# Performance work log

Hardware: AMD Instinct MI355X
Metric: run time of the kernel (lower is better)

## Reference

```python
import jax, jax.numpy as jnp
import numpy as np

EMBED_DIMS = 256
NUM_GROUPS = 8
NUM_LEVELS = 4
NUM_CAMS = 6
NUM_LEARNABLE_PTS = 6
FIX_SCALE = np.array([[0,0,0],[0.45,0,0],[-0.45,0,0],[0,0.45,0],[0,-0.45,0],[0,0,0.45],[0,0,-0.45]], dtype=np.float32)
NUM_PTS = len(FIX_SCALE) + NUM_LEARNABLE_PTS  # 13
GROUP_DIMS = EMBED_DIMS // NUM_GROUPS


def safe_sigmoid(x):
    return jax.nn.sigmoid(jnp.clip(x, -9.21, 9.21))


def get_rotation_matrix(q):
    # q: [..., 4] quaternion (w, x, y, z), normalized first (GaussianFormer convention)
    q = q / jnp.linalg.norm(q, axis=-1, keepdims=True)
    w, x, y, z = q[..., 0], q[..., 1], q[..., 2], q[..., 3]
    R = jnp.stack([
        jnp.stack([1 - 2 * (y * y + z * z), 2 * (x * y - w * z), 2 * (x * z + w * y)], axis=-1),
        jnp.stack([2 * (x * y + w * z), 1 - 2 * (x * x + z * z), 2 * (y * z - w * x)], axis=-1),
        jnp.stack([2 * (x * z - w * y), 2 * (y * z + w * x), 1 - 2 * (x * x + y * y)], axis=-1),
    ], axis=-2)
    return R  # [..., 3, 3]


def key_points_generator(anchor, instance_feature, W_learn, b_learn):
    bs, num_anchor = anchor.shape[:2]
    fix_scale = jnp.asarray(FIX_SCALE, anchor.dtype)  # [7, 3]
    scale = jnp.broadcast_to(fix_scale[None, None], (bs, num_anchor, fix_scale.shape[0], 3))
    learnable = safe_sigmoid((instance_feature @ W_learn + b_learn)
                             .reshape(bs, num_anchor, NUM_LEARNABLE_PTS, 3)) - 0.5
    scale = jnp.concatenate([scale, learnable], axis=-2)         # [bs, na, P, 3]
    gs_scales = anchor[..., None, 3:6]                           # [bs, na, 1, 3]
    key_points = scale * gs_scales                               # [bs, na, P, 3]
    rot_T = jnp.swapaxes(get_rotation_matrix(anchor[..., 6:10]), -1, -2)  # [bs, na, 3, 3]
    key_points = jnp.einsum('bnij,bnpj->bnpi', rot_T, key_points)
    return key_points + anchor[..., None, :3]                    # [bs, na, P, 3]


def project_points(key_points, projection_mat, image_wh):
    # key_points [bs, na, P, 3], projection_mat [bs, cams, 4, 4]
    ones = jnp.ones_like(key_points[..., :1])
    pts4 = jnp.concatenate([key_points, ones], axis=-1)          # [bs, na, P, 4]
    p2d = jnp.einsum('bcij,bnpj->bcnpi', projection_mat, pts4)   # [bs, cams, na, P, 4]
    p2d = p2d[..., :2] / jnp.maximum(p2d[..., 2:3], 1e-5)
    p2d = p2d / image_wh[:, :, None, None]
    return jnp.clip(p2d, 0.0, 0.9999)                            # [bs, cams, na, P, 2]


def bilinear_sample(feat, pts):
    # feat [bs, cams, C, H, W], pts [bs, P, cams, 2] normalized to [0,1]
    bs, cams, C, H, W = feat.shape
    x = pts[..., 0] * W - 0.5
    y = pts[..., 1] * H - 0.5
    x0 = jnp.floor(x); y0 = jnp.floor(y)
    wx = x - x0; wy = y - y0
    x0i = x0.astype(jnp.int32); y0i = y0.astype(jnp.int32)
    feat_f = jnp.transpose(feat, (0, 1, 3, 4, 2)).reshape(bs, cams, H * W, C)
    b_idx = jnp.arange(bs)[:, None, None]
    c_idx = jnp.arange(cams)[None, None, :]

    def gather(yy, xx):
        valid = (yy >= 0) & (yy < H) & (xx >= 0) & (xx < W)
        yc = jnp.clip(yy, 0, H - 1)
        xc = jnp.clip(xx, 0, W - 1)
        v = feat_f[b_idx, c_idx, yc * W + xc]                    # [bs, P, cams, C]
        return v * valid[..., None].astype(v.dtype)

    v00 = gather(y0i, x0i)
    v01 = gather(y0i, x0i + 1)
    v10 = gather(y0i + 1, x0i)
    v11 = gather(y0i + 1, x0i + 1)
    wx = wx[..., None]; wy = wy[..., None]
    return (v00 * (1 - wx) * (1 - wy) + v01 * wx * (1 - wy)
            + v10 * (1 - wx) * wy + v11 * wx * wy)               # [bs, P, cams, C]


def deformable_aggregate(feature_maps, points_2d, weights):
    # points_2d [bs, P, cams, 2]; weights [bs, P, cams, levels, groups]
    bs, P = points_2d.shape[:2]
    out = jnp.zeros((bs, P, NUM_GROUPS, GROUP_DIMS), points_2d.dtype)
    for l, feat in enumerate(feature_maps):
        samp = bilinear_sample(feat, points_2d)                  # [bs, P, cams, C]
        samp = samp.reshape(bs, P, feat.shape[1], NUM_GROUPS, GROUP_DIMS)
        out = out + jnp.einsum('bpcgd,bpcg->bpgd', samp, weights[:, :, :, l, :])
    return out.reshape(bs, P, EMBED_DIMS)


def _forward(pts3d, instance_feature, anchor, feat0, feat1, feat2, feat3,
             projection_mat, image_wh, W_learn, b_learn, W_wts, b_wts, W_out, b_out):
    bs, num_anchor = instance_feature.shape[:2]
    key_points = key_points_generator(anchor, instance_feature, W_learn, b_learn)
    # softmax weights over cams*levels*pts jointly, per group
    w = (instance_feature @ W_wts + b_wts).reshape(bs, num_anchor, -1, NUM_GROUPS)
    w = jax.nn.softmax(w, axis=-2)
    w = w.reshape(bs, num_anchor, NUM_CAMS, NUM_LEVELS, NUM_PTS, NUM_GROUPS)
    w = jnp.transpose(w, (0, 1, 4, 2, 3, 5)).reshape(bs, num_anchor * NUM_PTS, NUM_CAMS, NUM_LEVELS, NUM_GROUPS)
    p2d = project_points(key_points, projection_mat, image_wh)   # [bs, cams, na, P, 2]
    p2d = jnp.transpose(p2d, (0, 2, 3, 1, 4)).reshape(bs, num_anchor * NUM_PTS, NUM_CAMS, 2)
    feats = deformable_aggregate([feat0, feat1, feat2, feat3], p2d, w)
    feats = feats.reshape(bs, num_anchor, NUM_PTS, EMBED_DIMS).sum(axis=2)
    output = feats @ W_out + b_out
    return output + instance_feature


def setup_inputs() -> dict:
    key = jax.random.key(0)
    ks = jax.random.split(key, 16)
    bs, na = 1, 4096
    shapes = [(bs, 6, 256, 64, 176), (bs, 6, 256, 32, 88), (bs, 6, 256, 16, 44), (bs, 6, 256, 8, 22)]
    inp = {
        'pts3d': jax.random.normal(ks[0], (100000, 3), jnp.float32),
        'instance_feature': jax.random.normal(ks[1], (bs, na, EMBED_DIMS), jnp.float32),
        'anchor': jax.random.normal(ks[2], (bs, na, 11), jnp.float32),
        'feat0': jax.random.normal(ks[3], shapes[0], jnp.float32),
        'feat1': jax.random.normal(ks[4], shapes[1], jnp.float32),
        'feat2': jax.random.normal(ks[5], shapes[2], jnp.float32),
        'feat3': jax.random.normal(ks[6], shapes[3], jnp.float32),
        'projection_mat': jax.random.normal(ks[7], (bs, NUM_CAMS, 4, 4), jnp.float32),
        'image_wh': jnp.broadcast_to(jnp.array([704.0, 256.0], jnp.float32), (bs, NUM_CAMS, 2)),
        'W_learn': jax.random.normal(ks[8], (EMBED_DIMS, NUM_LEARNABLE_PTS * 3), jnp.float32) * 0.02,
        'b_learn': jnp.zeros((NUM_LEARNABLE_PTS * 3,), jnp.float32),
        'W_wts': jax.random.normal(ks[9], (EMBED_DIMS, NUM_GROUPS * NUM_CAMS * NUM_LEVELS * NUM_PTS), jnp.float32) * 0.02,
        'b_wts': jnp.zeros((NUM_GROUPS * NUM_CAMS * NUM_LEVELS * NUM_PTS,), jnp.float32),
        'W_out': jax.random.normal(ks[10], (EMBED_DIMS, EMBED_DIMS), jnp.float32) * 0.02,
        'b_out': jnp.zeros((EMBED_DIMS,), jnp.float32),
    }
    return inp


def reference(pts3d, instance_feature, anchor, feat0, feat1, feat2, feat3,
              projection_mat, image_wh, W_learn, b_learn, W_wts, b_wts, W_out, b_out):
    return _forward(pts3d, instance_feature, anchor, feat0, feat1, feat2, feat3,
                    projection_mat, image_wh, W_learn, b_learn, W_wts, b_wts, W_out, b_out)
```

## Files before the change

### kernel.cpp

```cpp
#include <hip/hip_runtime.h>
#include <math.h>


#define FT_L0 0
#define FT_L1 17301504
#define FT_L2 21626880
#define FT_L3 22708224
#define WS_LOGB 5744640
#define WS_FEATB 10856448
#define WS_LEARN 11380736
#define WS_AB 11454464
#define WS_BB 11978752
#define WS_WOB 12306432
#define WS_BIASP 12339200

typedef float v2f __attribute__((ext_vector_type(2)));
typedef __attribute__((ext_vector_type(8))) short bf16x8;
typedef __attribute__((ext_vector_type(4))) float f32x4;

__device__ const float FIXS[7][3] = {
    {0.f, 0.f, 0.f},  {0.45f, 0.f, 0.f}, {-0.45f, 0.f, 0.f}, {0.f, 0.45f, 0.f},
    {0.f, -0.45f, 0.f}, {0.f, 0.f, 0.45f}, {0.f, 0.f, -0.45f}};

__device__ __forceinline__ unsigned int f2bf(float f) {
  unsigned int u = __float_as_uint(f);
  u += 0x7fffu + ((u >> 16) & 1u);
  return u >> 16;
}
__device__ __forceinline__ float bf2f(unsigned short u) {
  return __uint_as_float(((unsigned int)u) << 16);
}

__global__ __launch_bounds__(256) void k_stage(
    const float* __restrict__ f0, const float* __restrict__ f1,
    const float* __restrict__ f2, const float* __restrict__ f3,
    unsigned char* __restrict__ featF,
    const float* __restrict__ iw, const float* __restrict__ Ww,
    const float* __restrict__ Wl, const float* __restrict__ Wo,
    const float* __restrict__ b_wts,
    unsigned short* __restrict__ Ab, unsigned short* __restrict__ Bb,
    unsigned short* __restrict__ Wob, float* __restrict__ biasP) {
  __shared__ unsigned short smu[32][33];
  const int tid = threadIdx.x;
  const int bid = blockIdx.x;
  if (bid < 2688) {
    const int bx7 = bid % 7;
    const int y = (bid / 7) & 63;
    const int c = bid / 448;
    const float* src;
    unsigned char* dst;
    int H, W, xt;
    if (bx7 < 3)      { src = f0; dst = featF + FT_L0; H = 64; W = 176; xt = bx7 * 64; }
    else if (bx7 < 5) { src = f1; dst = featF + FT_L1; H = 32; W = 88;  xt = (bx7 - 3) * 64; }
    else if (bx7 < 6) { src = f2; dst = featF + FT_L2; H = 16; W = 44;  xt = 0; }
    else              { src = f3; dst = featF + FT_L3; H = 8;  W = 22;  xt = 0; }
    if (y >= H) return;
    const int x = xt + (tid & 31) * 2;
    if (x >= W) return;
    const int q8 = tid >> 5;
    const int HW = H * W;
    const float* sp = src + ((c * 256 + q8 * 32) * H + y) * W + x;
    float2 v[32];
#pragma unroll
    for (int k = 0; k < 32; ++k) v[k] = *(const float2*)(sp + k * HW);
    __builtin_amdgcn_sched_barrier(0);
    unsigned int r0[8], r1[8];
#pragma unroll
    for (int k8 = 0; k8 < 8; ++k8) {
      int pk = __builtin_amdgcn_cvt_pk_fp8_f32(v[k8 * 4 + 0].x, v[k8 * 4 + 1].x, 0, false);
      pk = __builtin_amdgcn_cvt_pk_fp8_f32(v[k8 * 4 + 2].x, v[k8 * 4 + 3].x, pk, true);
      r0[k8] = (unsigned int)pk;
      int pk1 = __builtin_amdgcn_cvt_pk_fp8_f32(v[k8 * 4 + 0].y, v[k8 * 4 + 1].y, 0, false);
      pk1 = __builtin_amdgcn_cvt_pk_fp8_f32(v[k8 * 4 + 2].y, v[k8 * 4 + 3].y, pk1, true);
      r1[k8] = (unsigned int)pk1;
    }
    unsigned char* drow = dst + (((c * H + y) * W + x) * 256) + q8 * 32;
    *(uint4*)(drow)            = make_uint4(r0[0], r0[1], r0[2], r0[3]);
    *(uint4*)(drow + 16)       = make_uint4(r0[4], r0[5], r0[6], r0[7]);
    *(uint4*)(drow + 256)      = make_uint4(r1[0], r1[1], r1[2], r1[3]);
    *(uint4*)(drow + 256 + 16) = make_uint4(r1[4], r1[5], r1[6], r1[7]);
    return;
  }
  const int bx = bid - 2688;
  if (bx < 1024) {
    const int i = bx * 256 + tid;
    const float4 v = ((const float4*)iw)[i];
    uint2 o;
    o.x = f2bf(v.x) | (f2bf(v.y) << 16);
    o.y = f2bf(v.z) | (f2bf(v.w) << 16);
    const int mtile = i >> 10;
    const int ml = (i >> 6) & 15;
    const int kk = (i & 63) >> 3;
    const int q = (i >> 1) & 3;
    const int jj = (i & 1) * 4;
    *(uint2*)&Ab[mtile * 4096 + kk * 512 + q * 128 + ml * 8 + jj] = o;
    return;
  }
  const int i = tid & 31;
  const int r = tid >> 5;
  const int bxb = bx - 1024;
  if (bxb < 640) {
    const int j0 = (bxb % 80) * 32;
    const int k0 = (bxb / 80) * 32;
#pragma unroll
    for (int rr = r; rr < 32; rr += 8) {
      const int k = k0 + rr, jc = j0 + i;
      float v = 0.f;
      if (jc < 2496) v = Ww[k * 2496 + jc];
      else if (jc < 2514) v = Wl[k * 18 + (jc - 2496)];
      smu[rr][i] = (unsigned short)f2bf(v);
    }
    __syncthreads();
    const int jn = tid >> 3;
    const int kq = tid & 7;
    const int jc = j0 + jn;
    if (jc < 2514) {
      int colp;
      if (jc < 2496) {
        const int g = jc & 7, s = jc >> 3;
        const int c = s / 52, r2 = s - c * 52;
        const int l = r2 / 13, p = r2 - l * 13;
        colp = g * 312 + (p * 6 + c) * 4 + l;
      } else {
        colp = jc;
      }
      const int k = k0 + kq * 4;
      const int ntile = colp >> 4, mln = colp & 15;
      const int kkn = k >> 5, qn = (k >> 3) & 3, jj = k & 7;
      unsigned int h0 = (unsigned int)smu[kq * 4 + 0][jn] |
                        ((unsigned int)smu[kq * 4 + 1][jn] << 16);
      unsigned int h1 = (unsigned int)smu[kq * 4 + 2][jn] |
                        ((unsigned int)smu[kq * 4 + 3][jn] << 16);
      *(uint2*)&Bb[ntile * 4096 + kkn * 512 + qn * 128 + mln * 8 + jj] =
          make_uint2(h0, h1);
    }
    return;
  }
  const int bxw = bxb - 640;
  if (bxw < 64) {
    const int j0 = (bxw & 7) * 32;
    const int k0 = (bxw >> 3) * 32;
#pragma unroll
    for (int rr = r; rr < 32; rr += 8)
      smu[rr][i] = (unsigned short)f2bf(Wo[(k0 + rr) * 256 + j0 + i]);
    __syncthreads();
#pragma unroll
    for (int rr = r; rr < 32; rr += 8)
      Wob[(j0 + rr) * 256 + k0 + i] = smu[i][rr];
    return;
  }
  {
    const int jcol = (bxw - 64) * 256 + tid;
    if (jcol < 2496) {
      const int g = jcol & 7, s = jcol >> 3;
      const int c = s / 52, r2 = s - c * 52;
      const int l = r2 / 13, p = r2 - l * 13;
      biasP[g * 312 + (p * 6 + c) * 4 + l] = b_wts[jcol];
    }
  }
}

__global__ __launch_bounds__(256) void k_wts_mfma(
    const unsigned short* __restrict__ Ab, const unsigned short* __restrict__ Bb,
    const float* __restrict__ biasP, const float* __restrict__ b_learn,
    unsigned short* __restrict__ logitsP, float* __restrict__ learn) {
  __shared__ __align__(16) unsigned short t64[64][88];
  const int tid = threadIdx.x;
  const int w = tid >> 6, lane = tid & 63;
  const int ml = lane & 15, q = lane >> 4;
  const int n0 = blockIdx.x * 64;
  const int m0 = blockIdx.y * 64;
  f32x4 acc[4] = {{0.f, 0.f, 0.f, 0.f}, {0.f, 0.f, 0.f, 0.f},
                  {0.f, 0.f, 0.f, 0.f}, {0.f, 0.f, 0.f, 0.f}};
  const unsigned short* Ap = Ab + (blockIdx.y * 4 + w) * 4096 + lane * 8;
  const unsigned short* Bp = Bb + blockIdx.x * 4 * 4096 + lane * 8;
#pragma unroll
  for (int kk = 0; kk < 8; ++kk) {
    const bf16x8 a = *(const bf16x8*)(Ap + kk * 512);
#pragma unroll
    for (int nt = 0; nt < 4; ++nt) {
      const bf16x8 b = *(const bf16x8*)(Bp + nt * 4096 + kk * 512);
      acc[nt] = __builtin_amdgcn_mfma_f32_16x16x32_bf16(a, b, acc[nt], 0, 0, 0);
    }
  }
  if (blockIdx.x < 39) {
    const int wr = w * 16 + q * 4;
#pragma unroll
    for (int nt = 0; nt < 4; ++nt) {
      const float b = biasP[n0 + nt * 16 + ml];
#pragma unroll
      for (int r = 0; r < 4; ++r)
        t64[wr + r][nt * 16 + ml] = (unsigned short)f2bf(acc[nt][r] + b);
    }
    __syncthreads();
    const int row = tid >> 2, cq = tid & 3;
    unsigned short* drow = logitsP + (m0 + row) * 2496 + n0;
    *(uint4*)(drow + cq * 8) = *(const uint4*)&t64[row][cq * 8];
    *(uint4*)(drow + 32 + cq * 8) = *(const uint4*)&t64[row][32 + cq * 8];
  } else {
    const int rowb = m0 + w * 16 + q * 4;
#pragma unroll
    for (int nt = 0; nt < 4; ++nt) {
      const int col = n0 + nt * 16 + ml;
      if (col < 2514) {
        const float b = b_learn[col - 2496];
#pragma unroll
        for (int r = 0; r < 4; ++r) {
          float v = fminf(fmaxf(acc[nt][r] + b, -9.21f), 9.21f);
          learn[(rowb + r) * 18 + (col - 2496)] = 1.f / (1.f + expf(-v)) - 0.5f;
        }
      }
    }
  }
}

__device__ __forceinline__ void fma16(const uint4 u, const float s, v2f* acc) {
  const v2f w = {s, s};
  acc[0] += __builtin_amdgcn_cvt_pk_f32_fp8((int)u.x, false) * w;
  acc[1] += __builtin_amdgcn_cvt_pk_f32_fp8((int)u.x, true) * w;
  acc[2] += __builtin_amdgcn_cvt_pk_f32_fp8((int)u.y, false) * w;
  acc[3] += __builtin_amdgcn_cvt_pk_f32_fp8((int)u.y, true) * w;
  acc[4] += __builtin_amdgcn_cvt_pk_f32_fp8((int)u.z, false) * w;
  acc[5] += __builtin_amdgcn_cvt_pk_f32_fp8((int)u.z, true) * w;
  acc[6] += __builtin_amdgcn_cvt_pk_f32_fp8((int)u.w, false) * w;
  acc[7] += __builtin_amdgcn_cvt_pk_f32_fp8((int)u.w, true) * w;
}

__global__ __launch_bounds__(256, 8) void k_sample(
    const float* __restrict__ anchor, const unsigned short* __restrict__ logitsP,
    const float* __restrict__ learn_g, const unsigned char* __restrict__ featF,
    const float* __restrict__ proj, const float* __restrict__ wh,
    unsigned short* __restrict__ featsB) {
  const int n = blockIdx.x;
  const int tid = threadIdx.x;
  const int lane = tid & 63;
  const int wave = tid >> 6;
  __shared__ __align__(16) unsigned short s_w[8 * 328];
  __shared__ float s_p2d[78][2];
  __shared__ float s_learn[18];
  __shared__ union SmpLds {
    struct { int4 off[320]; float4 wt[320]; } tab;
    float red[4][256];
  } u;

  {
    const uint4* lp = (const uint4*)(logitsP + (size_t)n * 2496);
    for (int i = tid; i < 312; i += 256) {
      const int g = i / 39;
      ((uint4*)s_w)[g * 41 + (i - g * 39)] = lp[i];
    }
  }
  if (tid < 64) s_w[(tid >> 3) * 328 + 312 + (tid & 7)] = 0;
  if (tid < 18) s_learn[tid] = learn_g[n * 18 + tid];
  __syncthreads();

#pragma unroll
  for (int gg = 0; gg < 2; ++gg) {
    unsigned short* row = &s_w[(wave * 2 + gg) * 328];
    float l[5];
    float mx = -1e30f;
#pragma unroll
    for (int i = 0; i < 5; ++i) {
      const int s = lane + i * 64;
      l[i] = (s < 312) ? bf2f(row[s]) : -1e30f;
      mx = fmaxf(mx, l[i]);
    }
    for (int off = 32; off; off >>= 1) mx = fmaxf(mx, __shfl_xor(mx, off));
    float sum = 0.f;
#pragma unroll
    for (int i = 0; i < 5; ++i) {
      l[i] = __expf(l[i] - mx);
      sum += l[i];
    }
    for (int off = 32; off; off >>= 1) sum += __shfl_xor(sum, off);
    const float inv = 1.f / sum;
#pragma unroll
    for (int i = 0; i < 5; ++i) {
      const int s = lane + i * 64;
      if (s < 312) row[s] = (unsigned short)f2bf(l[i] * inv);
    }
  }

  if (tid < 78) {
    const int p = tid / 6, c = tid % 6;
    const float* an = anchor + n * 11;
    float qw = an[6], qx = an[7], qy = an[8], qz = an[9];
    const float qinv = 1.f / sqrtf(qw * qw + qx * qx + qy * qy + qz * qz);
    qw *= qinv; qx *= qinv; qy *= qinv; qz *= qinv;
    const float R00 = 1.f - 2.f * (qy * qy + qz * qz), R01 = 2.f * (qx * qy - qw * qz), R02 = 2.f * (qx * qz + qw * qy);
    const float R10 = 2.f * (qx * qy + qw * qz), R11 = 1.f - 2.f * (qx * qx + qz * qz), R12 = 2.f * (qy * qz - qw * qx);
    const float R20 = 2.f * (qx * qz - qw * qy), R21 = 2.f * (qy * qz + qw * qx), R22 = 1.f - 2.f * (qx * qx + qy * qy);
    float s0, s1, s2;
    if (p < 7) {
      s0 = FIXS[p][0]; s1 = FIXS[p][1]; s2 = FIXS[p][2];
    } else {
      const int b = (p - 7) * 3;
      s0 = s_learn[b]; s1 = s_learn[b + 1]; s2 = s_learn[b + 2];
    }
    const float vx = s0 * an[3], vy = s1 * an[4], vz = s2 * an[5];
    const float kx = R00 * vx + R10 * vy + R20 * vz + an[0];
    const float ky = R01 * vx + R11 * vy + R21 * vz + an[1];
    const float kz = R02 * vx + R12 * vy + R22 * vz + an[2];
    const float* P = proj + c * 16;
    const float h0 = P[0] * kx + P[1] * ky + P[2] * kz + P[3];
    const float h1 = P[4] * kx + P[5] * ky + P[6] * kz + P[7];
    const float h2 = P[8] * kx + P[9] * ky + P[10] * kz + P[11];
    const float zz = fmaxf(h2, 1e-5f);
    float px = h0 / zz / wh[c * 2 + 0];
    float py = h1 / zz / wh[c * 2 + 1];
    px = fminf(fmaxf(px, 0.f), 0.9999f);
    py = fminf(fmaxf(py, 0.f), 0.9999f);
    s_p2d[tid][0] = px;
    s_p2d[tid][1] = py;
  }
  __syncthreads();

  {
    constexpr int LBB[4] = {FT_L0, FT_L1, FT_L2, FT_L3};
    constexpr int CSB[4] = {2883584, 720896, 180224, 45056};
    for (int t = tid; t < 320; t += 256) {
      const int pc = t >> 2, l = t & 3;
      if (pc >= 78) {
        u.tab.off[t] = make_int4(0, 0, 0, 0);
        u.tab.wt[t] = make_float4(0.f, 0.f, 0.f, 0.f);
        continue;
      }
      const int c = pc % 6;
      const int H = 64 >> l, W = 176 >> l;
      const float fx = s_p2d[pc][0] * (float)W - 0.5f;
      const float fy = s_p2d[pc][1] * (float)H - 0.5f;
      const float x0f = floorf(fx), y0f = floorf(fy);
      const float wx = fx - x0f, wy = fy - y0f;
      const int x0 = (int)x0f, y0 = (int)y0f;
      const float mx0 = (x0 >= 0) ? 1.f : 0.f;
      const float mx1 = (x0 + 1 < W) ? 1.f : 0.f;
      const float my0 = (y0 >= 0) ? 1.f : 0.f;
      const float my1 = (y0 + 1 < H) ? 1.f : 0.f;
      const int cx0 = max(x0, 0), cx1 = min(x0 + 1, W - 1);
      const int cy0 = max(y0, 0), cy1 = min(y0 + 1, H - 1);
      const int base = LBB[l] + c * CSB[l];
      int4 o;
      o.x = base + (cy0 * W + cx0) * 256;
      o.y = base + (cy0 * W + cx1) * 256;
      o.z = base + (cy1 * W + cx0) * 256;
      o.w = base + (cy1 * W + cx1) * 256;
      u.tab.off[t] = o;
      float4 w4;
      w4.x = (1.f - wx) * (1.f - wy) * mx0 * my0;
      w4.y = wx * (1.f - wy) * mx1 * my0;
      w4.z = (1.f - wx) * wy * mx0 * my1;
      w4.w = wx * wy * mx1 * my1;
      u.tab.wt[t] = w4;
    }
  }
  __syncthreads();

  const int q = lane >> 4;
  const int ql = lane & 15;
  const int chb = ql * 16;
  const int g = ql >> 1;
  v2f acc[8];
#pragma unroll
  for (int k = 0; k < 8; ++k) acc[k] = (v2f){0.f, 0.f};
  const unsigned char* fbl = featF + chb;
  const unsigned short* wrow = &s_w[g * 328];
  const int pcb = wave * 4 + q;
#pragma unroll
  for (int it = 0; it < 5; ++it) {
    const int pc = pcb + it * 16;
    const int t0 = pc * 4;
    const uint2 wq = *(const uint2*)&wrow[t0];
    float wgl[4];
    wgl[0] = __uint_as_float(wq.x << 16);
    wgl[1] = __uint_as_float(wq.x & 0xffff0000u);
    wgl[2] = __uint_as_float(wq.y << 16);
    wgl[3] = __uint_as_float(wq.y & 0xffff0000u);
#pragma unroll
    for (int l4 = 0; l4 < 4; ++l4) {
      const int t = t0 + l4;
      const int4 o = u.tab.off[t];
      const float4 bw = u.tab.wt[t];
      const float wg = wgl[l4];
      const uint4 u0 = *(const uint4*)(fbl + o.x);
      const uint4 u1 = *(const uint4*)(fbl + o.y);
      const uint4 u2 = *(const uint4*)(fbl + o.z);
      const uint4 u3 = *(const uint4*)(fbl + o.w);
      fma16(u0, bw.x * wg, acc);
      fma16(u1, bw.y * wg, acc);
      fma16(u2, bw.z * wg, acc);
      fma16(u3, bw.w * wg, acc);
    }
  }
#pragma unroll
  for (int k = 0; k < 8; ++k) {
    v2f b;
    b.x = __shfl_xor(acc[k].x, 16);
    b.y = __shfl_xor(acc[k].y, 16);
    acc[k] += b;
    b.x = __shfl_xor(acc[k].x, 32);
    b.y = __shfl_xor(acc[k].y, 32);
    acc[k] += b;
  }
  __syncthreads();
  if (lane < 16) {
    float* dst = &u.red[wave][ql * 16];
    *(float4*)(dst + 0)  = make_float4(acc[0].x, acc[0].y, acc[1].x, acc[1].y);
    *(float4*)(dst + 4)  = make_float4(acc[2].x, acc[2].y, acc[3].x, acc[3].y);
    *(float4*)(dst + 8)  = make_float4(acc[4].x, acc[4].y, acc[5].x, acc[5].y);
    *(float4*)(dst + 12) = make_float4(acc[6].x, acc[6].y, acc[7].x, acc[7].y);
  }
  __syncthreads();
  {
    const float sum = u.red[0][tid] + u.red[1][tid] + u.red[2][tid] + u.red[3][tid];
    featsB[n * 256 + tid] = (unsigned short)f2bf(sum);
  }
}

__global__ __launch_bounds__(256) void k_out_mfma(
    const unsigned short* __restrict__ Ab, const unsigned short* __restrict__ Bb,
    const float* __restrict__ bias, const float* __restrict__ resid,
    float* __restrict__ out) {
  const int tid = threadIdx.x;
  const int w = tid >> 6, lane = tid & 63;
  const int ml = lane & 15, q = lane >> 4;
  const int n0 = blockIdx.x * 64;
  const int m0 = blockIdx.y * 64;
  f32x4 acc[4] = {{0.f, 0.f, 0.f, 0.f}, {0.f, 0.f, 0.f, 0.f},
                  {0.f, 0.f, 0.f, 0.f}, {0.f, 0.f, 0.f, 0.f}};
  const unsigned short* Ap = Ab + (m0 + w * 16 + ml) * 256 + q * 8;
  const unsigned short* Bp = Bb + (n0 + ml) * 256 + q * 8;
#pragma unroll
  for (int kk = 0; kk < 8; ++kk) {
    const bf16x8 a = *(const bf16x8*)(Ap + kk * 32);
#pragma unroll
    for (int nt = 0; nt < 4; ++nt) {
      const bf16x8 b = *(const bf16x8*)(Bp + nt * 16 * 256 + kk * 32);
      acc[nt] = __builtin_amdgcn_mfma_f32_16x16x32_bf16(a, b, acc[nt], 0, 0, 0);
    }
  }
  const int rowb = m0 + w * 16 + q * 4;
#pragma unroll
  for (int nt = 0; nt < 4; ++nt) {
    const int col = n0 + nt * 16 + ml;
    const float b = bias[col];
#pragma unroll
    for (int r = 0; r < 4; ++r) {
      const int row = rowb + r;
      out[row * 256 + col] = acc[nt][r] + b + resid[row * 256 + col];
    }
  }
}

extern "C" void kernel_launch(void* const* d_in, const int* in_sizes, int n_in,
                              void* d_out, int out_size, void* d_ws, size_t ws_size,
                              hipStream_t stream) {
  (void)in_sizes; (void)n_in; (void)out_size; (void)ws_size;
  const float* iw      = (const float*)d_in[1];
  const float* anchor  = (const float*)d_in[2];
  const float* f0      = (const float*)d_in[3];
  const float* f1      = (const float*)d_in[4];
  const float* f2      = (const float*)d_in[5];
  const float* f3      = (const float*)d_in[6];
  const float* proj    = (const float*)d_in[7];
  const float* wh      = (const float*)d_in[8];
  const float* W_learn = (const float*)d_in[9];
  const float* b_learn = (const float*)d_in[10];
  const float* W_wts   = (const float*)d_in[11];
  const float* b_wts   = (const float*)d_in[12];
  const float* W_out   = (const float*)d_in[13];
  const float* b_out   = (const float*)d_in[14];
  float* out = (float*)d_out;
  float* ws = (float*)d_ws;
  unsigned char*  featF   = (unsigned char*)ws;
  unsigned short* logitsP = (unsigned short*)(ws + WS_LOGB);
  unsigned short* featsB  = (unsigned short*)(ws + WS_FEATB);
  float*          learn   = ws + WS_LEARN;
  unsigned short* Ab      = (unsigned short*)(ws + WS_AB);
  unsigned short* Bb      = (unsigned short*)(ws + WS_BB);
  unsigned short* Wob     = (unsigned short*)(ws + WS_WOB);
  float*          biasP   = ws + WS_BIASP;

  k_stage<<<4427, 256, 0, stream>>>(f0, f1, f2, f3, featF, iw, W_wts, W_learn,
                                    W_out, b_wts, Ab, Bb, Wob, biasP);
  k_wts_mfma<<<dim3(40, 64), 256, 0, stream>>>(Ab, Bb, biasP, b_learn, logitsP, learn);
  k_sample<<<4096, 256, 0, stream>>>(anchor, logitsP, learn, featF, proj, wh, featsB);
  k_out_mfma<<<dim3(4, 64), 256, 0, stream>>>(featsB, Wob, b_out, iw, out);
}
```

Baseline: 246.0 us.

## Fuse output projection GEMM into sampling kernel per anchor

Removes the separate output-projection MFMA kernel and its bf16 feature round-trip through global memory. Each sampling block now does its own 1x256 by 256x256 product with MFMA, feeding zeros into 15 of the 16 A rows. The cost is that every block reads the full bf16 W_out (128 KB) from cache, and most of the MFMA work is wasted. It also adds LDS and a barrier, and the epilogue may raise register pressure and lower occupancy.

```diff
diff --git a/kernel.cpp b/kernel.cpp
--- a/kernel.cpp
+++ b/kernel.cpp
@@ -230,7 +230,8 @@
     const float* __restrict__ anchor, const unsigned short* __restrict__ logitsP,
     const float* __restrict__ learn_g, const unsigned char* __restrict__ featF,
     const float* __restrict__ proj, const float* __restrict__ wh,
-    unsigned short* __restrict__ featsB) {
+    const unsigned short* __restrict__ Wob, const float* __restrict__ b_out,
+    const float* __restrict__ resid, float* __restrict__ out) {
   const int n = blockIdx.x;
   const int tid = threadIdx.x;
   const int lane = tid & 63;
@@ -238,6 +239,7 @@
   __shared__ __align__(16) unsigned short s_w[8 * 328];
   __shared__ float s_p2d[78][2];
   __shared__ float s_learn[18];
+  __shared__ __align__(16) unsigned short s_feats[256];
   __shared__ union SmpLds {
     struct { int4 off[320]; float4 wt[320]; } tab;
     float red[4][256];
@@ -412,41 +414,33 @@
   __syncthreads();
   {
     const float sum = u.red[0][tid] + u.red[1][tid] + u.red[2][tid] + u.red[3][tid];
-    featsB[n * 256 + tid] = (unsigned short)f2bf(sum);
-  }
-}
-
-__global__ __launch_bounds__(256) void k_out_mfma(
-    const unsigned short* __restrict__ Ab, const unsigned short* __restrict__ Bb,
-    const float* __restrict__ bias, const float* __restrict__ resid,
-    float* __restrict__ out) {
-  const int tid = threadIdx.x;
-  const int w = tid >> 6, lane = tid & 63;
-  const int ml = lane & 15, q = lane >> 4;
-  const int n0 = blockIdx.x * 64;
-  const int m0 = blockIdx.y * 64;
-  f32x4 acc[4] = {{0.f, 0.f, 0.f, 0.f}, {0.f, 0.f, 0.f, 0.f},
-                  {0.f, 0.f, 0.f, 0.f}, {0.f, 0.f, 0.f, 0.f}};
-  const unsigned short* Ap = Ab + (m0 + w * 16 + ml) * 256 + q * 8;
-  const unsigned short* Bp = Bb + (n0 + ml) * 256 + q * 8;
-#pragma unroll
-  for (int kk = 0; kk < 8; ++kk) {
-    const bf16x8 a = *(const bf16x8*)(Ap + kk * 32);
-#pragma unroll
-    for (int nt = 0; nt < 4; ++nt) {
-      const bf16x8 b = *(const bf16x8*)(Bp + nt * 16 * 256 + kk * 32);
-      acc[nt] = __builtin_amdgcn_mfma_f32_16x16x32_bf16(a, b, acc[nt], 0, 0, 0);
-    }
-  }
-  const int rowb = m0 + w * 16 + q * 4;
-#pragma unroll
-  for (int nt = 0; nt < 4; ++nt) {
-    const int col = n0 + nt * 16 + ml;
-    const float b = bias[col];
-#pragma unroll
-    for (int r = 0; r < 4; ++r) {
-      const int row = rowb + r;
-      out[row * 256 + col] = acc[nt][r] + b + resid[row * 256 + col];
+    s_feats[tid] = (unsigned short)f2bf(sum);
+  }
+  __syncthreads();
+
+  {
+    const int ml = lane & 15;
+    f32x4 oacc[4] = {{0.f, 0.f, 0.f, 0.f}, {0.f, 0.f, 0.f, 0.f},
+                     {0.f, 0.f, 0.f, 0.f}, {0.f, 0.f, 0.f, 0.f}};
+    const unsigned short* Bp = Wob + (wave * 64 + ml) * 256 + q * 8;
+    const bf16x8 az = {0, 0, 0, 0, 0, 0, 0, 0};
+#pragma unroll
+    for (int kk = 0; kk < 8; ++kk) {
+      const bf16x8 a =
+          (ml == 0) ? *(const bf16x8*)&s_feats[kk * 32 + q * 8] : az;
+#pragma unroll
+      for (int nt = 0; nt < 4; ++nt) {
+        const bf16x8 b = *(const bf16x8*)(Bp + nt * 16 * 256 + kk * 32);
+        oacc[nt] = __builtin_amdgcn_mfma_f32_16x16x32_bf16(a, b, oacc[nt], 0, 0, 0);
+      }
+    }
+    if (lane < 16) {
+#pragma unroll
+      for (int nt = 0; nt < 4; ++nt) {
+        const int col = wave * 64 + nt * 16 + ml;
+        out[(size_t)n * 256 + col] =
+            oacc[nt][0] + b_out[col] + resid[(size_t)n * 256 + col];
+      }
     }
   }
 }
@@ -473,7 +467,6 @@
   float* ws = (float*)d_ws;
   unsigned char*  featF   = (unsigned char*)ws;
   unsigned short* logitsP = (unsigned short*)(ws + WS_LOGB);
-  unsigned short* featsB  = (unsigned short*)(ws + WS_FEATB);
   float*          learn   = ws + WS_LEARN;
   unsigned short* Ab      = (unsigned short*)(ws + WS_AB);
   unsigned short* Bb      = (unsigned short*)(ws + WS_BB);
@@ -483,6 +476,6 @@
   k_stage<<<4427, 256, 0, stream>>>(f0, f1, f2, f3, featF, iw, W_wts, W_learn,
                                     W_out, b_wts, Ab, Bb, Wob, biasP);
   k_wts_mfma<<<dim3(40, 64), 256, 0, stream>>>(Ab, Bb, biasP, b_learn, logitsP, learn);
-  k_sample<<<4096, 256, 0, stream>>>(anchor, logitsP, learn, featF, proj, wh, featsB);
-  k_out_mfma<<<dim3(4, 64), 256, 0, stream>>>(featsB, Wob, b_out, iw, out);
-}
+  k_sample<<<4096, 256, 0, stream>>>(anchor, logitsP, learn, featF, proj, wh,
+                                     Wob, b_out, iw, out);
+}
```

New measurement: 282.4 us. +14.8%, slower.
